# Kernel tuning notes

Measured on AMD Instinct MI355X. Metric: run time of the kernel, lower is better.

The kernel has to match this reference:

```python
import jax, jax.numpy as jnp
from jax import lax
import numpy as np

B, C, N, MAX_OUT = 8, 16, 2048, 100


def setup_inputs() -> dict:
    key = jax.random.key(0)
    kc, kw, ks = jax.random.split(key, 3)
    # well-formed xyxy boxes: centers in [0,1000), sizes in [1,101)
    ctr = jax.random.uniform(kc, (B, N, 2), jnp.float32) * 1000.0
    wh = jax.random.uniform(kw, (B, N, 2), jnp.float32) * 100.0 + 1.0
    boxes = jnp.concatenate([ctr - wh * 0.5, ctr + wh * 0.5], axis=-1)  # [B,N,4]
    scores = jax.random.uniform(ks, (B, C, N), jnp.float32)  # [B,C,N]
    return {
        "boxes": boxes,
        "scores": scores,
        "max_output_boxes_per_class": MAX_OUT,
        "iou_threshold": jnp.array([0.5], jnp.float32),
        "score_threshold": jnp.array([0.5], jnp.float32),
    }


def _pairwise_iou(bx):
    # bx: [N,4] xyxy -> [N,N] IoU (matches torchvision.ops.box_iou)
    x1, y1, x2, y2 = bx[:, 0], bx[:, 1], bx[:, 2], bx[:, 3]
    area = (x2 - x1) * (y2 - y1)
    iw = jnp.clip(jnp.minimum(x2[:, None], x2[None, :]) - jnp.maximum(x1[:, None], x1[None, :]), 0.0)
    ih = jnp.clip(jnp.minimum(y2[:, None], y2[None, :]) - jnp.maximum(y1[:, None], y1[None, :]), 0.0)
    inter = iw * ih
    return inter / (area[:, None] + area[None, :] - inter)


def _nms_selected(boxes, scores, iou_threshold, score_threshold, max_out):
    # boxes [B,N,4], scores [B,C,N]
    b, c, n = scores.shape
    iou = jax.vmap(_pairwise_iou)(boxes)  # [B,N,N], shared across classes
    iou_t = iou_threshold.reshape(())
    score_t = score_threshold.reshape(())

    def one_class(iou_b, cls_scores):
        order = jnp.argsort(-cls_scores)          # descending score order [N]
        valid = cls_scores[order] > score_t       # strict >, as in the torch code

        def step(suppressed, inp):
            ok, bi = inp
            kept = ok & (~suppressed[bi])
            # greedy suppression: a kept box removes all boxes with IoU > thr
            suppressed = suppressed | (kept & (iou_b[bi] > iou_t))
            return suppressed, kept

        _, keep = lax.scan(step, jnp.zeros((n,), bool), (valid, order))
        rank = jnp.cumsum(keep.astype(jnp.int32)) - 1
        sel = keep & (rank < max_out)
        pos = jnp.where(sel, rank, max_out)  # overflow/non-selected -> dropped slot
        buf = jnp.full((max_out + 1,), -1, jnp.int32).at[pos].set(
            jnp.where(sel, order.astype(jnp.int32), -1))
        return buf[:max_out]  # box indices in score order, -1 padded

    per_bc = jax.vmap(lambda iou_b, sb: jax.vmap(lambda s: one_class(iou_b, s))(sb))(iou, scores)  # [B,C,max_out]
    b_idx = jnp.broadcast_to(jnp.arange(b, dtype=jnp.int32)[:, None, None], per_bc.shape)
    c_idx = jnp.broadcast_to(jnp.arange(c, dtype=jnp.int32)[None, :, None], per_bc.shape)
    rows = jnp.stack([b_idx, c_idx, per_bc], axis=-1).reshape(-1, 3)  # [B*C*max_out, 3]
    # invalid (padded) rows are all -1
    return jnp.where(rows[:, 2:3] >= 0, rows, -1)


def reference(boxes, scores, max_output_boxes_per_class, iou_threshold, score_threshold):
    return _nms_selected(boxes, scores, iou_threshold, score_threshold,
                         int(max_output_boxes_per_class))
```

## Files before the change

kernel.cpp:

```cpp
#include <hip/hip_runtime.h>
#include <stdint.h>


#define NBOX 2048
#define HALF 1024
#define TA 512
#define TB 1024
#define CHUNK 128
#define MAXKEEP 256

typedef unsigned long long u64;

__device__ __forceinline__ unsigned flipf(float s) {
  unsigned b = __float_as_uint(s);
  return (b & 0x80000000u) ? ~b : (b | 0x80000000u);
}

__device__ __forceinline__ u64 ce_x(u64 v, int s, bool up, int lane) {
  u64 p = __shfl_xor(v, s, 64);
  bool lower = ((lane & s) == 0);
  u64 mx = v > p ? v : p;
  u64 mn = v > p ? p : v;
  return (up == lower) ? mx : mn;
}

__global__ __launch_bounds__(TA) void sort_half_kernel(
    const float* __restrict__ scores, u64* __restrict__ wsKeys, int C)
{
  __shared__ u64 sk[HALF];
  const int tid = threadIdx.x, lane = tid & 63, w = tid >> 6;
  const int bc = blockIdx.x >> 1;
  const int h  = blockIdx.x & 1;
  const float* cls = scores + (size_t)bc * NBOX + h * HALF;

  const int p0 = w * 128 + lane;
  const int p1 = p0 + 64;
  const int g0 = h * HALF + p0, g1 = h * HALF + p1;
  u64 e0 = ((u64)flipf(cls[p0]) << 32) | (0xFFFFFFFFu - (unsigned)g0);
  u64 e1 = ((u64)flipf(cls[p1]) << 32) | (0xFFFFFFFFu - (unsigned)g1);

  #pragma unroll
  for (int k = 2; k <= 64; k <<= 1) {
    #pragma unroll
    for (int s = k >> 1; s >= 1; s >>= 1) {
      bool up0 = ((lane & k) == 0);
      bool up1 = (((64 + lane) & k) == 0);
      e0 = ce_x(e0, s, up0, lane);
      e1 = ce_x(e1, s, up1, lane);
    }
  }
  {
    bool up = ((w & 1) == 0);
    u64 mx = e0 > e1 ? e0 : e1, mn = e0 > e1 ? e1 : e0;
    e0 = up ? mx : mn; e1 = up ? mn : mx;
    #pragma unroll
    for (int s = 32; s >= 1; s >>= 1) {
      e0 = ce_x(e0, s, up, lane);
      e1 = ce_x(e1, s, up, lane);
    }
  }
  sk[p0] = e0; sk[p1] = e1;
  __syncthreads();

  for (int k = 256; k <= HALF; k <<= 1) {
    for (int s = k >> 1; s >= 128; s >>= 1) {
      unsigned i = ((tid & ~(s - 1)) << 1) | (tid & (s - 1));
      unsigned j = i | (unsigned)s;
      u64 a = sk[i], bb = sk[j];
      bool up = ((i & (unsigned)k) == 0);
      bool sw = up ? (a < bb) : (a > bb);
      if (sw) { sk[i] = bb; sk[j] = a; }
      __syncthreads();
    }
    e0 = sk[p0]; e1 = sk[p1];
    bool up = (((unsigned)p0 & (unsigned)k) == 0);
    u64 mx = e0 > e1 ? e0 : e1, mn = e0 > e1 ? e1 : e0;
    e0 = up ? mx : mn; e1 = up ? mn : mx;
    #pragma unroll
    for (int s = 32; s >= 1; s >>= 1) {
      e0 = ce_x(e0, s, up, lane);
      e1 = ce_x(e1, s, up, lane);
    }
    if (k < HALF) { sk[p0] = e0; sk[p1] = e1; __syncthreads(); }
  }

  u64* dst = wsKeys + (size_t)bc * NBOX + h * HALF;
  if (h == 0) { dst[p0] = e0; dst[p1] = e1; }
  else        { dst[HALF - 1 - p0] = e0; dst[HALF - 1 - p1] = e1; }
}

__global__ __launch_bounds__(TB) void nms_kernel(
    const float* __restrict__ boxes,
    const u64* __restrict__ wsKeys,
    const int* __restrict__ maxOutPtr,
    const float* __restrict__ iouThrPtr,
    const float* __restrict__ scoreThrPtr,
    int* __restrict__ out, int B, int C, int slots)
{
  __shared__ u64 sk[NBOX];
  __shared__ float sx1[NBOX], sy1[NBOX], sx2[NBOX], sy2[NBOX], sar[NBOX];
  __shared__ unsigned colmask[CHUNK][4];
  __shared__ unsigned char suppPre[CHUNK];
  __shared__ int keptPos[MAXKEEP];
  __shared__ int Vsh, cntSh;

  const int tid = threadIdx.x, lane = tid & 63, w = tid >> 6;
  const int bc = blockIdx.x;
  const int b = bc / C, c = bc % C;
  const float iouT = iouThrPtr[0];
  const unsigned thrU = flipf(scoreThrPtr[0]);
  int mOut = maxOutPtr[0];
  if (mOut > slots) mOut = slots;
  if (mOut > MAXKEEP) mOut = MAXKEEP;
  if (mOut < 0) mOut = 0;

  if (tid == 0) { Vsh = 0; cntSh = 0; }

  const u64* src = wsKeys + (size_t)bc * NBOX;
  u64 v0 = src[tid], v1 = src[tid + HALF];
  sk[tid] = v0; sk[tid + HALF] = v1;
  int pop = __popcll(__ballot((unsigned)(v0 >> 32) > thrU)) +
            __popcll(__ballot((unsigned)(v1 >> 32) > thrU));
  __syncthreads();
  if (lane == 0) atomicAdd(&Vsh, pop);

  for (int s = 1024; s >= 128; s >>= 1) {
    unsigned i = ((tid & ~(s - 1)) << 1) | (tid & (s - 1));
    unsigned j = i | (unsigned)s;
    u64 a = sk[i], bb = sk[j];
    if (a < bb) { sk[i] = bb; sk[j] = a; }
    __syncthreads();
  }
  {
    const int j0 = w * 128 + lane, j1 = j0 + 64;
    u64 e0 = sk[j0], e1 = sk[j1];
    u64 mx = e0 > e1 ? e0 : e1, mn = e0 > e1 ? e1 : e0;
    e0 = mx; e1 = mn;
    #pragma unroll
    for (int s = 32; s >= 1; s >>= 1) {
      e0 = ce_x(e0, s, true, lane);
      e1 = ce_x(e1, s, true, lane);
    }
    sk[j0] = e0; sk[j1] = e1;
  }
  __syncthreads();
  const int V = Vsh;

  const float4* bx = (const float4*)boxes + (size_t)b * NBOX;
  for (int p = tid; p < V; p += TB) {
    int idx = (int)(0xFFFFFFFFu - (unsigned)sk[p]);
    float4 f = bx[idx];
    sx1[p] = f.x; sy1[p] = f.y; sx2[p] = f.z; sy2[p] = f.w;
    sar[p] = (f.z - f.x) * (f.w - f.y);
  }
  __syncthreads();

  int cnt = 0;
  for (int c0 = 0; c0 < V && cnt < mOut; c0 += CHUNK) {
    int clen = V - c0; if (clen > CHUNK) clen = CHUNK;

    if (tid < CHUNK * 4) ((unsigned*)colmask)[tid] = 0;
    if (tid < CHUNK) suppPre[tid] = 0;
    __syncthreads();

    {
      int qo = tid & (CHUNK - 1);
      int ko = tid >> 7;
      if (qo < clen) {
        int q = c0 + qo;
        float qx1 = sx1[q], qy1 = sy1[q], qx2 = sx2[q], qy2 = sy2[q], qa = sar[q];
        int hit = 0;
        for (int k = ko; k < cnt; k += 8) {
          int kp = keptPos[k];
          float iw = fminf(sx2[kp], qx2) - fmaxf(sx1[kp], qx1);
          float ih = fminf(sy2[kp], qy2) - fmaxf(sy1[kp], qy1);
          iw = fmaxf(iw, 0.0f); ih = fmaxf(ih, 0.0f);
          float inter = iw * ih;
          float iou = inter / (sar[kp] + qa - inter);
          if (iou > iouT) hit = 1;
        }
        if (hit) suppPre[qo] = 1;
      }
    }

    {
      int i = tid & (CHUNK - 1);
      if (i < clen) {
        int ip = c0 + i;
        float ix1 = sx1[ip], iy1 = sy1[ip], ix2 = sx2[ip], iy2 = sy2[ip], ia = sar[ip];
        for (int j = tid >> 7; j < clen; j += 8) {
          if (j <= i) continue;
          int q = c0 + j;
          float iw = fminf(ix2, sx2[q]) - fmaxf(ix1, sx1[q]);
          float ih = fminf(iy2, sy2[q]) - fmaxf(iy1, sy1[q]);
          iw = fmaxf(iw, 0.0f); ih = fmaxf(ih, 0.0f);
          float inter = iw * ih;
          float iou = inter / (ia + sar[q] - inter);
          if (iou > iouT) atomicOr(&colmask[j][i >> 5], 1u << (i & 31));
        }
      }
    }
    __syncthreads();

    if (w == 0) {
      unsigned a0 = colmask[lane][0], a1 = colmask[lane][1];
      unsigned b0 = colmask[lane + 64][0], b1 = colmask[lane + 64][1];
      unsigned b2 = colmask[lane + 64][2], b3 = colmask[lane + 64][3];
      bool supA = (lane < clen) ? (suppPre[lane] != 0) : true;
      bool supB = (lane + 64 < clen) ? (suppPre[lane + 64] != 0) : true;
      bool doneA = (lane >= clen);
      bool doneB = (lane + 64 >= clen);
      int cl = cnt;
      while (cl < mOut) {
        u64 cand = __ballot(!doneA && !supA);
        if (!cand) break;
        int r = __ffsll((long long)cand) - 1;
        if (lane == 0) keptPos[cl] = c0 + r;
        cl++;
        if (lane == r) doneA = true;
        unsigned av = (r < 32) ? a0 : a1;
        unsigned bv = (r < 32) ? b0 : b1;
        unsigned bit = (unsigned)r & 31;
        supA = supA || ((av >> bit) & 1);
        supB = supB || ((bv >> bit) & 1);
      }
      while (cl < mOut) {
        u64 cand = __ballot(!doneB && !supB);
        if (!cand) break;
        int r = __ffsll((long long)cand) - 1;
        if (lane == 0) keptPos[cl] = c0 + 64 + r;
        cl++;
        if (lane == r) doneB = true;
        unsigned bv = (r < 32) ? b2 : b3;
        unsigned bit = (unsigned)r & 31;
        supB = supB || ((bv >> bit) & 1);
      }
      if (lane == 0) cntSh = cl;
    }
    __syncthreads();
    cnt = cntSh;
  }

  int base = bc * slots * 3;
  for (int s = tid; s < slots; s += TB) {
    int v = -1;
    if (s < cnt) {
      int p = keptPos[s];
      v = (int)(0xFFFFFFFFu - (unsigned)sk[p]);
    }
    out[base + s * 3 + 0] = (v >= 0) ? b : -1;
    out[base + s * 3 + 1] = (v >= 0) ? c : -1;
    out[base + s * 3 + 2] = v;
  }
}

extern "C" void kernel_launch(void* const* d_in, const int* in_sizes, int n_in,
                              void* d_out, int out_size, void* d_ws, size_t ws_size,
                              hipStream_t stream) {
  const float* boxes  = (const float*)d_in[0];
  const float* scores = (const float*)d_in[1];
  const int*   maxOut = (const int*)d_in[2];
  const float* iouT   = (const float*)d_in[3];
  const float* scoreT = (const float*)d_in[4];
  int* out = (int*)d_out;
  u64* wsKeys = (u64*)d_ws;

  const int N = NBOX;
  int B = in_sizes[0] / (4 * N);
  int C = in_sizes[1] / (B * N);
  int slots = out_size / (B * C * 3);

  sort_half_kernel<<<dim3(B * C * 2), dim3(TA), 0, stream>>>(scores, wsKeys, C);
  nms_kernel<<<dim3(B * C), dim3(TB), 0, stream>>>(
      boxes, wsKeys, maxOut, iouT, scoreT, out, B, C, slots);
}
```

Measured before the change: 89.57 us.

## Replace in-kernel bitonic merge with merge-path merge of sorted halves

```diff
diff --git a/kernel.cpp b/kernel.cpp
--- a/kernel.cpp
+++ b/kernel.cpp
@@ -5,7 +5,7 @@
 #define NBOX 2048
 #define HALF 1024
 #define TA 512
-#define TB 1024
+#define TB 512
 #define CHUNK 128
 #define MAXKEEP 256
 
@@ -85,8 +85,7 @@
   }
 
   u64* dst = wsKeys + (size_t)bc * NBOX + h * HALF;
-  if (h == 0) { dst[p0] = e0; dst[p1] = e1; }
-  else        { dst[HALF - 1 - p0] = e0; dst[HALF - 1 - p1] = e1; }
+  dst[p0] = e0; dst[p1] = e1;
 }
 
 __global__ __launch_bounds__(TB) void nms_kernel(
@@ -97,7 +96,8 @@
     const float* __restrict__ scoreThrPtr,
     int* __restrict__ out, int B, int C, int slots)
 {
-  __shared__ u64 sk[NBOX];
+  __shared__ u64 rk[NBOX];
+  __shared__ int sidx[NBOX];
   __shared__ float sx1[NBOX], sy1[NBOX], sx2[NBOX], sy2[NBOX], sar[NBOX];
   __shared__ unsigned colmask[CHUNK][4];
   __shared__ unsigned char suppPre[CHUNK];
@@ -117,41 +117,48 @@
   if (tid == 0) { Vsh = 0; cntSh = 0; }
 
   const u64* src = wsKeys + (size_t)bc * NBOX;
-  u64 v0 = src[tid], v1 = src[tid + HALF];
-  sk[tid] = v0; sk[tid + HALF] = v1;
-  int pop = __popcll(__ballot((unsigned)(v0 >> 32) > thrU)) +
-            __popcll(__ballot((unsigned)(v1 >> 32) > thrU));
+  int pop = 0;
+  #pragma unroll
+  for (int p = 0; p < NBOX; p += TB) {
+    u64 v = src[p + tid];
+    rk[p + tid] = v;
+    pop += __popcll(__ballot((unsigned)(v >> 32) > thrU));
+  }
+  if (tid < CHUNK * 4) ((unsigned*)colmask)[tid] = 0;
+  if (tid < CHUNK) suppPre[tid] = 0;
   __syncthreads();
   if (lane == 0) atomicAdd(&Vsh, pop);
-
-  for (int s = 1024; s >= 128; s >>= 1) {
-    unsigned i = ((tid & ~(s - 1)) << 1) | (tid & (s - 1));
-    unsigned j = i | (unsigned)s;
-    u64 a = sk[i], bb = sk[j];
-    if (a < bb) { sk[i] = bb; sk[j] = a; }
-    __syncthreads();
-  }
+  __syncthreads();
+  const int V = Vsh;
+
   {
-    const int j0 = w * 128 + lane, j1 = j0 + 64;
-    u64 e0 = sk[j0], e1 = sk[j1];
-    u64 mx = e0 > e1 ? e0 : e1, mn = e0 > e1 ? e1 : e0;
-    e0 = mx; e1 = mn;
-    #pragma unroll
-    for (int s = 32; s >= 1; s >>= 1) {
-      e0 = ce_x(e0, s, true, lane);
-      e1 = ce_x(e1, s, true, lane);
-    }
-    sk[j0] = e0; sk[j1] = e1;
-  }
-  __syncthreads();
-  const int V = Vsh;
-
-  const float4* bx = (const float4*)boxes + (size_t)b * NBOX;
-  for (int p = tid; p < V; p += TB) {
-    int idx = (int)(0xFFFFFFFFu - (unsigned)sk[p]);
-    float4 f = bx[idx];
-    sx1[p] = f.x; sy1[p] = f.y; sx2[p] = f.z; sy2[p] = f.w;
-    sar[p] = (f.z - f.x) * (f.w - f.y);
+    const u64* r0 = rk;
+    const u64* r1 = rk + HALF;
+    int d = tid * 4;
+    int lo = d - HALF; if (lo < 0) lo = 0;
+    int hi = d < HALF ? d : HALF;
+    while (lo < hi) {
+      int a = (lo + hi) >> 1;
+      if (r0[a] > r1[d - a - 1]) lo = a + 1; else hi = a;
+    }
+    int a = lo, bb = d - lo;
+    const float4* bx = (const float4*)boxes + (size_t)b * NBOX;
+    #pragma unroll
+    for (int q = 0; q < 4; ++q) {
+      u64 v0 = (a < HALF) ? r0[a] : 0;
+      u64 v1 = (bb < HALF) ? r1[bb] : 0;
+      bool take0 = (bb >= HALF) || ((a < HALF) && (v0 > v1));
+      u64 v = take0 ? v0 : v1;
+      if (take0) a++; else bb++;
+      int p = d + q;
+      int idx = (int)(0xFFFFFFFFu - (unsigned)v);
+      sidx[p] = idx;
+      if (p < V) {
+        float4 f = bx[idx];
+        sx1[p] = f.x; sy1[p] = f.y; sx2[p] = f.z; sy2[p] = f.w;
+        sar[p] = (f.z - f.x) * (f.w - f.y);
+      }
+    }
   }
   __syncthreads();
 
@@ -159,9 +166,11 @@
   for (int c0 = 0; c0 < V && cnt < mOut; c0 += CHUNK) {
     int clen = V - c0; if (clen > CHUNK) clen = CHUNK;
 
-    if (tid < CHUNK * 4) ((unsigned*)colmask)[tid] = 0;
-    if (tid < CHUNK) suppPre[tid] = 0;
-    __syncthreads();
+    if (c0 > 0) {
+      if (tid < CHUNK * 4) ((unsigned*)colmask)[tid] = 0;
+      if (tid < CHUNK) suppPre[tid] = 0;
+      __syncthreads();
+    }
 
     {
       int qo = tid & (CHUNK - 1);
@@ -170,7 +179,7 @@
         int q = c0 + qo;
         float qx1 = sx1[q], qy1 = sy1[q], qx2 = sx2[q], qy2 = sy2[q], qa = sar[q];
         int hit = 0;
-        for (int k = ko; k < cnt; k += 8) {
+        for (int k = ko; k < cnt; k += 4) {
           int kp = keptPos[k];
           float iw = fminf(sx2[kp], qx2) - fmaxf(sx1[kp], qx1);
           float ih = fminf(sy2[kp], qy2) - fmaxf(sy1[kp], qy1);
@@ -188,7 +197,7 @@
       if (i < clen) {
         int ip = c0 + i;
         float ix1 = sx1[ip], iy1 = sy1[ip], ix2 = sx2[ip], iy2 = sy2[ip], ia = sar[ip];
-        for (int j = tid >> 7; j < clen; j += 8) {
+        for (int j = tid >> 7; j < clen; j += 4) {
           if (j <= i) continue;
           int q = c0 + j;
           float iw = fminf(ix2, sx2[q]) - fmaxf(ix1, sx1[q]);
@@ -243,11 +252,7 @@
 
   int base = bc * slots * 3;
   for (int s = tid; s < slots; s += TB) {
-    int v = -1;
-    if (s < cnt) {
-      int p = keptPos[s];
-      v = (int)(0xFFFFFFFFu - (unsigned)sk[p]);
-    }
+    int v = (s < cnt) ? sidx[keptPos[s]] : -1;
     out[base + s * 3 + 0] = (v >= 0) ? b : -1;
     out[base + s * 3 + 1] = (v >= 0) ? c : -1;
     out[base + s * 3 + 2] = v;
```

After: 90.85 us. No clear change (+1.4%).
